# Kernel optimization log

Measured on AMD Instinct MI355X. Metric: run time of the kernel, lower is better.

The kernel has to match this reference:

```python
import jax, jax.numpy as jnp
import numpy as np

NUM_NODES = 100000
NUM_EDGES = 1200000
DIM = 64
NUM_LAYERS = 3
NUM_GRAPHS = 512
BN_EPS = 1e-5


def setup_inputs() -> dict:
    key = jax.random.key(0)
    ks = jax.random.split(key, 12)
    x = jax.random.normal(ks[0], (NUM_NODES, DIM), dtype=jnp.float32)
    edge_index = jax.random.randint(ks[1], (2, NUM_EDGES), 0, NUM_NODES, dtype=jnp.int64)
    edge_weight = jax.random.uniform(ks[2], (NUM_EDGES,), dtype=jnp.float32)
    batch = jnp.sort(jax.random.randint(ks[3], (NUM_NODES,), 0, NUM_GRAPHS, dtype=jnp.int64))
    W1 = jax.random.normal(ks[4], (NUM_LAYERS, DIM, DIM), dtype=jnp.float32) * 0.1
    b1 = jax.random.normal(ks[5], (NUM_LAYERS, DIM), dtype=jnp.float32) * 0.1
    W2 = jax.random.normal(ks[6], (NUM_LAYERS, DIM, DIM), dtype=jnp.float32) * 0.1
    b2 = jax.random.normal(ks[7], (NUM_LAYERS, DIM), dtype=jnp.float32) * 0.1
    gamma = jax.random.uniform(ks[8], (NUM_LAYERS, DIM), dtype=jnp.float32) + 0.5
    beta = jax.random.normal(ks[9], (NUM_LAYERS, DIM), dtype=jnp.float32) * 0.1
    return {"x": x, "edge_index": edge_index, "edge_weight": edge_weight,
            "batch": batch, "pool": 0, "W1": W1, "b1": b1, "W2": W2,
            "b2": b2, "gamma": gamma, "beta": beta}


def reference(x, edge_index, edge_weight, batch, pool, W1, b1, W2, b2, gamma, beta):
    # WGINConv (eps=0): h = MLP(x + scatter_add(edge_weight * x[src] -> dst))
    # then ReLU, then BatchNorm1d in training mode (batch statistics).
    src, dst = edge_index[0], edge_index[1]
    n_nodes = x.shape[0]
    xs = []
    for i in range(W1.shape[0]):
        msg = x[src] * edge_weight[:, None]                       # [E, D] gather
        agg = jax.ops.segment_sum(msg, dst, num_segments=n_nodes)  # [N, D] scatter-add
        h = agg + x                                                # (1+eps)*x, eps=0
        h = jax.nn.relu(h @ W1[i].T + b1[i]) @ W2[i].T + b2[i]     # GIN MLP
        h = jax.nn.relu(h)
        mu = h.mean(0)
        var = ((h - mu) ** 2).mean(0)                              # biased var (BN train)
        x = gamma[i] * (h - mu) * jax.lax.rsqrt(var + BN_EPS) + beta[i]
        xs.append(x)
    if pool == 0:  # 'add' pooling (static python int)
        xpool = [jax.ops.segment_sum(v, batch, num_segments=NUM_GRAPHS) for v in xs]
    else:          # 'mean' pooling
        counts = jax.ops.segment_sum(jnp.ones((n_nodes,), x.dtype), batch,
                                     num_segments=NUM_GRAPHS)
        denom = jnp.maximum(counts, 1.0)[:, None]
        xpool = [jax.ops.segment_sum(v, batch, num_segments=NUM_GRAPHS) / denom for v in xs]
    return (jnp.concatenate(xpool, axis=1), jnp.concatenate(xs, axis=1))
```

## Files before the change

kernel.cpp:

```cpp
#include <hip/hip_runtime.h>

#define N_NODES 100000
#define N_EDGES 1200000
#define DIM     64
#define N_LAYERS 3
#define N_GRAPHS 512
#define OUTD    192
#define BN_EPS  1e-5f

#define NPB 64
#define LDS_PITCH 65
#define NLBLK ((N_NODES + NPB - 1) / NPB)

#define BSHIFT 9
#define BUCK_NODES (1 << BSHIFT)
#define NBUK ((N_NODES + BUCK_NODES - 1) / BUCK_NODES)
#define EPB 4096
#define NPBLK ((N_EDGES + EPB - 1) / EPB)

__global__ void transpose_w(const float* __restrict__ W1, const float* __restrict__ W2,
                            float* __restrict__ W1T, float* __restrict__ W2T,
                            float* __restrict__ idaff) {
    int idx = blockIdx.x * blockDim.x + threadIdx.x;
    if (idx < 128) idaff[idx] = (idx < 64) ? 1.0f : 0.0f;
    if (idx >= N_LAYERS * DIM * DIM) return;
    int l = idx >> 12;
    int r = idx & 4095;
    int j = r >> 6;
    int k = r & 63;
    int dstp = (l << 12) + k * DIM + j;
    W1T[dstp] = W1[idx];
    W2T[dstp] = W2[idx];
}

__global__ void __launch_bounds__(256) part_hist(const int* __restrict__ dst,
                                                 int* __restrict__ hist) {
    __shared__ int h[NBUK];
    int t = threadIdx.x;
    if (t < NBUK) h[t] = 0;
    __syncthreads();
    int base = blockIdx.x * EPB;
    for (int i = t; i < EPB; i += 256) {
        int e = base + i;
        if (e < N_EDGES) atomicAdd(&h[dst[e] >> BSHIFT], 1);
    }
    __syncthreads();
    if (t < NBUK) hist[blockIdx.x * NBUK + t] = h[t];
}

__global__ void __launch_bounds__(256) part_scan(const int* __restrict__ hist,
                                                 int* __restrict__ base,
                                                 int* __restrict__ bstart) {
    __shared__ int tot[256];
    int b = threadIdx.x;
    int run = 0;
    if (b < NBUK) {
        for (int k = 0; k < NPBLK; ++k) {
            base[k * NBUK + b] = run;
            run += hist[k * NBUK + b];
        }
    }
    tot[b] = (b < NBUK) ? run : 0;
    __syncthreads();
    int v = tot[b];
    for (int o = 1; o < 256; o <<= 1) {
        int add = (b >= o) ? tot[b - o] : 0;
        __syncthreads();
        tot[b] += add;
        __syncthreads();
    }
    int excl = tot[b] - v;
    if (b < NBUK) {
        bstart[b] = excl;
        for (int k = 0; k < NPBLK; ++k) base[k * NBUK + b] += excl;
        if (b == NBUK - 1) bstart[NBUK] = excl + v;
    }
}

__global__ void __launch_bounds__(256) part_scatter(
        const int* __restrict__ src, const int* __restrict__ dst,
        const float* __restrict__ ew, const int* __restrict__ base,
        int2* __restrict__ pp) {
    __shared__ int cur[NBUK];
    int t = threadIdx.x;
    if (t < NBUK) cur[t] = base[blockIdx.x * NBUK + t];
    __syncthreads();
    int bb = blockIdx.x * EPB;
    for (int i = t; i < EPB; i += 256) {
        int e = bb + i;
        if (e < N_EDGES) {
            int d = dst[e];
            int bk = d >> BSHIFT;
            int pos = atomicAdd(&cur[bk], 1);
            int dl = d & (BUCK_NODES - 1);
            pp[pos] = make_int2(src[e] | (dl << 17), __float_as_int(ew[e]));
        }
    }
}

__global__ void __launch_bounds__(256) csr_build(
        const int2* __restrict__ pp, const int* __restrict__ bstart,
        int* __restrict__ seg, int2* __restrict__ pe) {
    __shared__ int cnt[BUCK_NODES];
    __shared__ int ssum[256];
    int b = blockIdx.x, t = threadIdx.x;
    int ebeg = bstart[b], eend = bstart[b + 1];
    cnt[t] = 0;
    cnt[t + 256] = 0;
    __syncthreads();
    for (int e = ebeg + t; e < eend; e += 256)
        atomicAdd(&cnt[pp[e].x >> 17], 1);
    __syncthreads();
    int c0 = cnt[2 * t], c1 = cnt[2 * t + 1];
    int ps = c0 + c1;
    ssum[t] = ps;
    __syncthreads();
    int v = ps;
    for (int o = 1; o < 256; o <<= 1) {
        int add = (t >= o) ? ssum[t - o] : 0;
        __syncthreads();
        ssum[t] += add;
        __syncthreads();
    }
    int excl = ssum[t] - v;
    int o0 = ebeg + excl;
    int o1 = o0 + c0;
    int n0 = (b << BSHIFT) + 2 * t;
    if (n0 < N_NODES) seg[n0] = o0;
    if (n0 + 1 < N_NODES) seg[n0 + 1] = o1;
    __syncthreads();
    cnt[2 * t] = o0;
    cnt[2 * t + 1] = o1;
    __syncthreads();
    for (int e = ebeg + t; e < eend; e += 256) {
        int2 p = pp[e];
        int pos = atomicAdd(&cnt[p.x >> 17], 1);
        pe[pos] = make_int2(p.x & 0x1FFFF, p.y);
    }
    if (b == 0 && t == 0) seg[N_NODES] = N_EDGES;
}

__global__ void __launch_bounds__(256) layer_kernel(
    const float* __restrict__ x_in, int xstride,
    const int* __restrict__ seg,
    const int2* __restrict__ pe,
    const float* __restrict__ affine ,
    const float* __restrict__ W1T, const float* __restrict__ b1,
    const float* __restrict__ W2T, const float* __restrict__ b2,
    float* __restrict__ out ,
    float* __restrict__ pstat ) {
    __shared__ float lds[NPB * LDS_PITCH];
    int t = threadIdx.x;
    int lane = t & 63;
    int wid = __builtin_amdgcn_readfirstlane(t >> 6);
    int nbase = blockIdx.x * NPB;

    float sc_in = affine[lane];
    float sh_in = affine[64 + lane];

    for (int nn = 0; nn < 16; ++nn) {
        int n = nbase + wid * 16 + nn;
        float acc = 0.0f;
        if (n < N_NODES) {
            int beg = seg[n];
            int end = seg[n + 1];
            float a0 = x_in[(size_t)n * xstride + lane];
            float a1 = 0.0f, a2 = 0.0f, a3 = 0.0f;
            float ws = 0.0f;
            int e = beg;
            for (; e + 4 <= end; e += 4) {
                int2 p0 = pe[e];
                int2 p1 = pe[e + 1];
                int2 p2 = pe[e + 2];
                int2 p3 = pe[e + 3];
                float w0 = __int_as_float(p0.y);
                float w1 = __int_as_float(p1.y);
                float w2 = __int_as_float(p2.y);
                float w3 = __int_as_float(p3.y);
                a0 = fmaf(w0, x_in[(size_t)p0.x * xstride + lane], a0);
                a1 = fmaf(w1, x_in[(size_t)p1.x * xstride + lane], a1);
                a2 = fmaf(w2, x_in[(size_t)p2.x * xstride + lane], a2);
                a3 = fmaf(w3, x_in[(size_t)p3.x * xstride + lane], a3);
                ws += (w0 + w1) + (w2 + w3);
            }
            for (; e < end; ++e) {
                int2 p = pe[e];
                float w = __int_as_float(p.y);
                a1 = fmaf(w, x_in[(size_t)p.x * xstride + lane], a1);
                ws += w;
            }
            acc = fmaf(sc_in, (a0 + a1) + (a2 + a3), sh_in * (1.0f + ws));
        }
        lds[(wid * 16 + nn) * LDS_PITCH + lane] = acc;
    }
    __syncthreads();

    float h[16];
#pragma unroll
    for (int jj = 0; jj < 16; ++jj) h[jj] = b1[wid * 16 + jj];
#pragma unroll 4
    for (int k = 0; k < DIM; ++k) {
        float xv = lds[lane * LDS_PITCH + k];
        const float* wr = W1T + k * DIM + wid * 16;
#pragma unroll
        for (int jj = 0; jj < 16; ++jj) h[jj] = fmaf(xv, wr[jj], h[jj]);
    }
#pragma unroll
    for (int jj = 0; jj < 16; ++jj) h[jj] = fmaxf(h[jj], 0.0f);
    __syncthreads();
#pragma unroll
    for (int jj = 0; jj < 16; ++jj) lds[lane * LDS_PITCH + wid * 16 + jj] = h[jj];
    __syncthreads();

    float o[16];
#pragma unroll
    for (int jj = 0; jj < 16; ++jj) o[jj] = b2[wid * 16 + jj];
#pragma unroll 4
    for (int k = 0; k < DIM; ++k) {
        float hv = lds[lane * LDS_PITCH + k];
        const float* wr = W2T + k * DIM + wid * 16;
#pragma unroll
        for (int jj = 0; jj < 16; ++jj) o[jj] = fmaf(hv, wr[jj], o[jj]);
    }
    int n = nbase + lane;
    bool valid = (n < N_NODES);
#pragma unroll
    for (int jj = 0; jj < 16; ++jj) o[jj] = fmaxf(o[jj], 0.0f);
    if (valid) {
        float* orow = out + (size_t)n * OUTD + wid * 16;
#pragma unroll
        for (int jj = 0; jj < 16; jj += 4) {
            *(float4*)(orow + jj) = make_float4(o[jj], o[jj + 1], o[jj + 2], o[jj + 3]);
        }
    }

    float my_s = 0.0f, my_q = 0.0f;
#pragma unroll
    for (int jj = 0; jj < 16; ++jj) {
        float v = valid ? o[jj] : 0.0f;
        float vs = v, vq = v * v;
#pragma unroll
        for (int m = 1; m < 64; m <<= 1) {
            vs += __shfl_xor(vs, m);
            vq += __shfl_xor(vq, m);
        }
        if (lane == jj) { my_s = vs; my_q = vq; }
    }
    if (lane < 16) {
        size_t base = (size_t)blockIdx.x * 128 + wid * 16 + lane;
        pstat[base] = my_s;
        pstat[base + 64] = my_q;
    }
}

__global__ void __launch_bounds__(256) reduce_stats(
    const float* __restrict__ pstat,
    const float* __restrict__ gamma, const float* __restrict__ beta,
    float* __restrict__ ss ) {
    __shared__ double part[16][16];
    int b = blockIdx.x;
    int t = threadIdx.x;
    int slot = t & 15;
    int g = t >> 4;
    int d = b * 8 + (slot & 7);
    int off = (slot < 8) ? 0 : 64;
    double s = 0.0;
    for (int blk = g; blk < NLBLK; blk += 16)
        s += (double)pstat[(size_t)blk * 128 + off + d];
    part[g][slot] = s;
    __syncthreads();
    if (t < 16) {
        double x = 0.0;
#pragma unroll
        for (int k = 0; k < 16; ++k) x += part[k][t];
        part[0][t] = x;
    }
    __syncthreads();
    if (t < 8) {
        int dd = b * 8 + t;
        double mu = part[0][t] / (double)N_NODES;
        double var = part[0][8 + t] / (double)N_NODES - mu * mu;
        float inv = (float)(1.0 / sqrt(var + (double)BN_EPS));
        float sc = gamma[dd] * inv;
        ss[dd] = sc;
        ss[64 + dd] = beta[dd] - (float)mu * sc;
    }
}

__global__ void bn_pool(float* __restrict__ xs,
                        const int* __restrict__ batch,
                        const float* __restrict__ ss ,
                        float* __restrict__ pooled) {
    int g = blockIdx.x;
    int part = blockIdx.y;
    int d = threadIdx.x;
    int l = d >> 6, dd = d & 63;
    float sc = ss[l * 128 + dd];
    float sh = ss[l * 128 + 64 + dd];
    int start, end;
    {
        int lo = 0, hi = N_NODES;
        while (lo < hi) { int m = (lo + hi) >> 1; if (batch[m] < g) lo = m + 1; else hi = m; }
        start = lo;
    }
    {
        int lo = start, hi = N_NODES;
        while (lo < hi) { int m = (lo + hi) >> 1; if (batch[m] <= g) lo = m + 1; else hi = m; }
        end = lo;
    }
    float acc = 0.0f;
    for (int n = start + part; n < end; n += 4) {
        float* p = xs + (size_t)n * OUTD + d;
        float v = fmaf(*p, sc, sh);
        *p = v;
        acc += v;
    }
    atomicAdd(&pooled[(size_t)g * OUTD + d], acc);
}

extern "C" void kernel_launch(void* const* d_in, const int* in_sizes, int n_in,
                              void* d_out, int out_size, void* d_ws, size_t ws_size,
                              hipStream_t stream) {
    const float* x0    = (const float*)d_in[0];
    const int*   ei    = (const int*)d_in[1];
    const float* ew    = (const float*)d_in[2];
    const int*   batch = (const int*)d_in[3];
    const float* W1    = (const float*)d_in[5];
    const float* b1    = (const float*)d_in[6];
    const float* W2    = (const float*)d_in[7];
    const float* b2    = (const float*)d_in[8];
    const float* gamma = (const float*)d_in[9];
    const float* beta  = (const float*)d_in[10];

    float* pooled = (float*)d_out;
    float* xs     = pooled + (size_t)N_GRAPHS * OUTD;

    const int* src = ei;
    const int* dst = ei + N_EDGES;

    int2*  pe     = (int2*)d_ws;
    int2*  pp     = pe + N_EDGES;
    int*   seg    = (int*)(pp + N_EDGES);
    int*   hist   = seg + N_NODES + 4;
    int*   pbase  = hist + (size_t)NPBLK * NBUK;
    int*   bstart = pbase + (size_t)NPBLK * NBUK;
    float* W1T    = (float*)(bstart + NBUK + 4);
    float* W2T    = W1T + N_LAYERS * DIM * DIM;
    float* idaff  = W2T + N_LAYERS * DIM * DIM;
    float* ss     = idaff + 128;
    float* pstat  = ss + N_LAYERS * 128;

    transpose_w<<<(N_LAYERS * DIM * DIM + 255) / 256, 256, 0, stream>>>(
        W1, W2, W1T, W2T, idaff);

    part_hist<<<NPBLK, 256, 0, stream>>>(dst, hist);
    part_scan<<<1, 256, 0, stream>>>(hist, pbase, bstart);
    part_scatter<<<NPBLK, 256, 0, stream>>>(src, dst, ew, pbase, pp);
    csr_build<<<NBUK, 256, 0, stream>>>(pp, bstart, seg, pe);

    for (int i = 0; i < N_LAYERS; ++i) {
        const float* xin = (i == 0) ? x0 : (xs + (size_t)(i - 1) * DIM);
        int xstride = (i == 0) ? DIM : OUTD;
        const float* affine = (i == 0) ? idaff : (ss + (size_t)(i - 1) * 128);

        layer_kernel<<<NLBLK, 256, 0, stream>>>(
            xin, xstride, seg, pe, affine,
            W1T + (size_t)i * DIM * DIM, b1 + (size_t)i * DIM,
            W2T + (size_t)i * DIM * DIM, b2 + (size_t)i * DIM,
            xs + (size_t)i * DIM, pstat);

        reduce_stats<<<8, 256, 0, stream>>>(
            pstat, gamma + (size_t)i * DIM, beta + (size_t)i * DIM,
            ss + (size_t)i * 128);
    }

    hipMemsetAsync(pooled, 0, (size_t)N_GRAPHS * OUTD * sizeof(float), stream);
    dim3 pgrid(N_GRAPHS, 4);
    bn_pool<<<pgrid, OUTD, 0, stream>>>(xs, batch, ss, pooled);
}
```

Baseline: 558.5 us.

## Parallelize partition scan and stage block edge lists in LDS

Replaces the single-block serial scan over NPBLK×NBUK histogram entries with global atomic bucket totals, a small single-block scan, and a per-bucket parallel scan kernel that fills partition bases. The layer kernel now copies each block's contiguous edge range (up to 1280 edges) into LDS before gathering, falling back to global reads when the range does not fit. The gather loop is unrolled to 8 independent accumulators. The costs are extra LDS per block, which may lower occupancy, plus an added memset and an extra kernel launch.

```diff
diff --git a/kernel.cpp b/kernel.cpp
--- a/kernel.cpp
+++ b/kernel.cpp
@@ -11,6 +11,7 @@
 #define NPB 64
 #define LDS_PITCH 65
 #define NLBLK ((N_NODES + NPB - 1) / NPB)
+#define ECAP 1280
 
 #define BSHIFT 9
 #define BUCK_NODES (1 << BSHIFT)
@@ -34,7 +35,8 @@
 }
 
 __global__ void __launch_bounds__(256) part_hist(const int* __restrict__ dst,
-                                                 int* __restrict__ hist) {
+                                                 int* __restrict__ hist,
+                                                 int* __restrict__ tot) {
     __shared__ int h[NBUK];
     int t = threadIdx.x;
     if (t < NBUK) h[t] = 0;
@@ -45,36 +47,53 @@
         if (e < N_EDGES) atomicAdd(&h[dst[e] >> BSHIFT], 1);
     }
     __syncthreads();
-    if (t < NBUK) hist[blockIdx.x * NBUK + t] = h[t];
-}
-
-__global__ void __launch_bounds__(256) part_scan(const int* __restrict__ hist,
-                                                 int* __restrict__ base,
-                                                 int* __restrict__ bstart) {
-    __shared__ int tot[256];
-    int b = threadIdx.x;
-    int run = 0;
-    if (b < NBUK) {
-        for (int k = 0; k < NPBLK; ++k) {
-            base[k * NBUK + b] = run;
-            run += hist[k * NBUK + b];
-        }
-    }
-    tot[b] = (b < NBUK) ? run : 0;
-    __syncthreads();
-    int v = tot[b];
+    if (t < NBUK) {
+        int v = h[t];
+        hist[blockIdx.x * NBUK + t] = v;
+        if (v) atomicAdd(&tot[t], v);
+    }
+}
+
+__global__ void __launch_bounds__(256) scan196(const int* __restrict__ tot,
+                                               int* __restrict__ bstart) {
+    __shared__ int lds[256];
+    int t = threadIdx.x;
+    int v = (t < NBUK) ? tot[t] : 0;
+    lds[t] = v;
+    __syncthreads();
     for (int o = 1; o < 256; o <<= 1) {
-        int add = (b >= o) ? tot[b - o] : 0;
-        __syncthreads();
-        tot[b] += add;
-        __syncthreads();
-    }
-    int excl = tot[b] - v;
-    if (b < NBUK) {
-        bstart[b] = excl;
-        for (int k = 0; k < NPBLK; ++k) base[k * NBUK + b] += excl;
-        if (b == NBUK - 1) bstart[NBUK] = excl + v;
-    }
+        int add = (t >= o) ? lds[t - o] : 0;
+        __syncthreads();
+        lds[t] += add;
+        __syncthreads();
+    }
+    if (t < NBUK) bstart[t] = lds[t] - v;
+    if (t == 0) bstart[NBUK] = N_EDGES;
+}
+
+__global__ void __launch_bounds__(256) base_fill(const int* __restrict__ hist,
+                                                 const int* __restrict__ bstart,
+                                                 int* __restrict__ base) {
+    __shared__ int c[512];
+    __shared__ int ssum[256];
+    int b = blockIdx.x, t = threadIdx.x;
+    c[t] = (t < NPBLK) ? hist[t * NBUK + b] : 0;
+    c[t + 256] = (t + 256 < NPBLK) ? hist[(t + 256) * NBUK + b] : 0;
+    __syncthreads();
+    int c0 = c[2 * t], c1 = c[2 * t + 1];
+    int ps = c0 + c1;
+    ssum[t] = ps;
+    __syncthreads();
+    int v = ps;
+    for (int o = 1; o < 256; o <<= 1) {
+        int add = (t >= o) ? ssum[t - o] : 0;
+        __syncthreads();
+        ssum[t] += add;
+        __syncthreads();
+    }
+    int excl = ssum[t] - v + bstart[b];
+    if (2 * t < NPBLK)     base[(2 * t) * NBUK + b] = excl;
+    if (2 * t + 1 < NPBLK) base[(2 * t + 1) * NBUK + b] = excl + c0;
 }
 
 __global__ void __launch_bounds__(256) part_scatter(
@@ -150,46 +169,80 @@
     float* __restrict__ out ,
     float* __restrict__ pstat ) {
     __shared__ float lds[NPB * LDS_PITCH];
+    __shared__ int2 eds[ECAP];
     int t = threadIdx.x;
     int lane = t & 63;
     int wid = __builtin_amdgcn_readfirstlane(t >> 6);
     int nbase = blockIdx.x * NPB;
+    int nend = (nbase + NPB < N_NODES) ? nbase + NPB : N_NODES;
+
+    int eb = seg[nbase];
+    int ee = seg[nend];
+    int ne = ee - eb;
+    for (int i = t; i < ne && i < ECAP; i += 256) eds[i] = pe[eb + i];
 
     float sc_in = affine[lane];
     float sh_in = affine[64 + lane];
+    __syncthreads();
+    bool fit = (ne <= ECAP);
 
     for (int nn = 0; nn < 16; ++nn) {
         int n = nbase + wid * 16 + nn;
         float acc = 0.0f;
         if (n < N_NODES) {
-            int beg = seg[n];
-            int end = seg[n + 1];
+            int lbeg = seg[n] - eb;
+            int lend = seg[n + 1] - eb;
             float a0 = x_in[(size_t)n * xstride + lane];
             float a1 = 0.0f, a2 = 0.0f, a3 = 0.0f;
+            float a4 = 0.0f, a5 = 0.0f, a6 = 0.0f, a7 = 0.0f;
             float ws = 0.0f;
-            int e = beg;
-            for (; e + 4 <= end; e += 4) {
-                int2 p0 = pe[e];
-                int2 p1 = pe[e + 1];
-                int2 p2 = pe[e + 2];
-                int2 p3 = pe[e + 3];
-                float w0 = __int_as_float(p0.y);
-                float w1 = __int_as_float(p1.y);
-                float w2 = __int_as_float(p2.y);
-                float w3 = __int_as_float(p3.y);
-                a0 = fmaf(w0, x_in[(size_t)p0.x * xstride + lane], a0);
-                a1 = fmaf(w1, x_in[(size_t)p1.x * xstride + lane], a1);
-                a2 = fmaf(w2, x_in[(size_t)p2.x * xstride + lane], a2);
-                a3 = fmaf(w3, x_in[(size_t)p3.x * xstride + lane], a3);
-                ws += (w0 + w1) + (w2 + w3);
+            int e = lbeg;
+#define GATHER_BODY(FETCH)                                                     \
+            for (; e + 8 <= lend; e += 8) {                                    \
+                int2 p0 = FETCH(e);     int2 p1 = FETCH(e + 1);                \
+                int2 p2 = FETCH(e + 2); int2 p3 = FETCH(e + 3);                \
+                int2 p4 = FETCH(e + 4); int2 p5 = FETCH(e + 5);                \
+                int2 p6 = FETCH(e + 6); int2 p7 = FETCH(e + 7);                \
+                float w0 = __int_as_float(p0.y), w1 = __int_as_float(p1.y);    \
+                float w2 = __int_as_float(p2.y), w3 = __int_as_float(p3.y);    \
+                float w4 = __int_as_float(p4.y), w5 = __int_as_float(p5.y);    \
+                float w6 = __int_as_float(p6.y), w7 = __int_as_float(p7.y);    \
+                a0 = fmaf(w0, x_in[(size_t)p0.x * xstride + lane], a0);        \
+                a1 = fmaf(w1, x_in[(size_t)p1.x * xstride + lane], a1);        \
+                a2 = fmaf(w2, x_in[(size_t)p2.x * xstride + lane], a2);        \
+                a3 = fmaf(w3, x_in[(size_t)p3.x * xstride + lane], a3);        \
+                a4 = fmaf(w4, x_in[(size_t)p4.x * xstride + lane], a4);        \
+                a5 = fmaf(w5, x_in[(size_t)p5.x * xstride + lane], a5);        \
+                a6 = fmaf(w6, x_in[(size_t)p6.x * xstride + lane], a6);        \
+                a7 = fmaf(w7, x_in[(size_t)p7.x * xstride + lane], a7);        \
+                ws += ((w0 + w1) + (w2 + w3)) + ((w4 + w5) + (w6 + w7));       \
+            }                                                                  \
+            for (; e + 4 <= lend; e += 4) {                                    \
+                int2 p0 = FETCH(e);     int2 p1 = FETCH(e + 1);                \
+                int2 p2 = FETCH(e + 2); int2 p3 = FETCH(e + 3);                \
+                float w0 = __int_as_float(p0.y), w1 = __int_as_float(p1.y);    \
+                float w2 = __int_as_float(p2.y), w3 = __int_as_float(p3.y);    \
+                a0 = fmaf(w0, x_in[(size_t)p0.x * xstride + lane], a0);        \
+                a1 = fmaf(w1, x_in[(size_t)p1.x * xstride + lane], a1);        \
+                a2 = fmaf(w2, x_in[(size_t)p2.x * xstride + lane], a2);        \
+                a3 = fmaf(w3, x_in[(size_t)p3.x * xstride + lane], a3);        \
+                ws += (w0 + w1) + (w2 + w3);                                   \
+            }                                                                  \
+            for (; e < lend; ++e) {                                            \
+                int2 p = FETCH(e);                                             \
+                float w = __int_as_float(p.y);                                 \
+                a4 = fmaf(w, x_in[(size_t)p.x * xstride + lane], a4);          \
+                ws += w;                                                       \
             }
-            for (; e < end; ++e) {
-                int2 p = pe[e];
-                float w = __int_as_float(p.y);
-                a1 = fmaf(w, x_in[(size_t)p.x * xstride + lane], a1);
-                ws += w;
-            }
-            acc = fmaf(sc_in, (a0 + a1) + (a2 + a3), sh_in * (1.0f + ws));
+#define F_LDS(i) eds[i]
+#define F_GBL(i) pe[eb + (i)]
+            if (fit) { GATHER_BODY(F_LDS) }
+            else     { GATHER_BODY(F_GBL) }
+#undef F_LDS
+#undef F_GBL
+#undef GATHER_BODY
+            float s = ((a0 + a1) + (a2 + a3)) + ((a4 + a5) + (a6 + a7));
+            acc = fmaf(sc_in, s, sh_in * (1.0f + ws));
         }
         lds[(wid * 16 + nn) * LDS_PITCH + lane] = acc;
     }
@@ -343,7 +396,8 @@
     int*   seg    = (int*)(pp + N_EDGES);
     int*   hist   = seg + N_NODES + 4;
     int*   pbase  = hist + (size_t)NPBLK * NBUK;
-    int*   bstart = pbase + (size_t)NPBLK * NBUK;
+    int*   tot    = pbase + (size_t)NPBLK * NBUK;
+    int*   bstart = tot + NBUK + 4;
     float* W1T    = (float*)(bstart + NBUK + 4);
     float* W2T    = W1T + N_LAYERS * DIM * DIM;
     float* idaff  = W2T + N_LAYERS * DIM * DIM;
@@ -353,8 +407,10 @@
     transpose_w<<<(N_LAYERS * DIM * DIM + 255) / 256, 256, 0, stream>>>(
         W1, W2, W1T, W2T, idaff);
 
-    part_hist<<<NPBLK, 256, 0, stream>>>(dst, hist);
-    part_scan<<<1, 256, 0, stream>>>(hist, pbase, bstart);
+    hipMemsetAsync(tot, 0, (NBUK + 4) * sizeof(int), stream);
+    part_hist<<<NPBLK, 256, 0, stream>>>(dst, hist, tot);
+    scan196<<<1, 256, 0, stream>>>(tot, bstart);
+    base_fill<<<NBUK, 256, 0, stream>>>(hist, bstart, pbase);
     part_scatter<<<NPBLK, 256, 0, stream>>>(src, dst, ew, pbase, pp);
     csr_build<<<NBUK, 256, 0, stream>>>(pp, bstart, seg, pe);
 
```

Result: slower. 578.3 us (+3.5%).
